# Kernel optimization log

Measured on AMD Instinct MI355X. Metric: run time of the kernel, lower is better.

Reference implementation:

```python
import jax, jax.numpy as jnp
import numpy as np

B, H, W, C = 32, 56, 56, 192
WS, SHIFT, HEADS = 7, 3, 6
HID = 4 * C
N = WS * WS
NW = (H // WS) * (W // WS)
EPS = 1e-5


def _rel_index():
    ch, cw = np.meshgrid(np.arange(WS), np.arange(WS), indexing='ij')
    coords = np.stack([ch.ravel(), cw.ravel()])  # [2, N]
    rel = coords[:, :, None] - coords[:, None, :]  # [2, N, N]
    rel = rel.transpose(1, 2, 0)
    rel[:, :, 0] += WS - 1
    rel[:, :, 1] += WS - 1
    rel[:, :, 0] *= 2 * WS - 1
    return rel.sum(-1).astype(np.int32)  # [N, N]


def _attn_mask():
    img = np.zeros((H, W), np.float32)
    sl = (slice(0, -WS), slice(-WS, -SHIFT), slice(-SHIFT, None))
    cnt = 0
    for hs in sl:
        for ws_ in sl:
            img[hs, ws_] = cnt
            cnt += 1
    mw = img.reshape(H // WS, WS, W // WS, WS).transpose(0, 2, 1, 3).reshape(-1, N)
    m = mw[:, None, :] - mw[:, :, None]
    return np.where(m != 0, -100.0, 0.0).astype(np.float32)  # [NW, N, N]


def setup_inputs() -> dict:
    key = jax.random.key(0)
    ks = jax.random.split(key, 16)
    r = lambda k, s, sc: (jax.random.normal(k, s, jnp.float32) * sc)
    return {
        'x': r(ks[0], (B, H * W, C), 1.0),
        'norm1_w': jnp.ones((C,), jnp.float32),
        'norm1_b': jnp.zeros((C,), jnp.float32),
        'qkv_w': r(ks[1], (C, 3 * C), 0.02),
        'qkv_b': jnp.zeros((3 * C,), jnp.float32),
        'bias_table': r(ks[2], ((2 * WS - 1) ** 2, HEADS), 0.02),
        'proj_w': r(ks[3], (C, C), 0.02),
        'proj_b': jnp.zeros((C,), jnp.float32),
        'norm2_w': jnp.ones((C,), jnp.float32),
        'norm2_b': jnp.zeros((C,), jnp.float32),
        'fc1_w': r(ks[4], (C, HID), 0.02),
        'fc1_b': jnp.zeros((HID,), jnp.float32),
        'fc2_w': r(ks[5], (HID, C), 0.02),
        'fc2_b': jnp.zeros((C,), jnp.float32),
        'attn_mask': jnp.asarray(_attn_mask()),
        'rel_index': jnp.asarray(_rel_index()),
    }


def _ln(x, w, b):
    mu = jnp.mean(x, -1, keepdims=True)
    var = jnp.mean(jnp.square(x - mu), -1, keepdims=True)
    return (x - mu) * jax.lax.rsqrt(var + EPS) * w + b


def reference(x, norm1_w, norm1_b, qkv_w, qkv_b, bias_table, proj_w, proj_b,
              norm2_w, norm2_b, fc1_w, fc1_b, fc2_w, fc2_b, attn_mask, rel_index):
    shortcut = x
    h = _ln(x, norm1_w, norm1_b).reshape(B, H, W, C)
    # cyclic shift
    h = jnp.roll(h, shift=(-SHIFT, -SHIFT), axis=(1, 2))
    # window partition -> (B*NW, N, C)
    h = h.reshape(B, H // WS, WS, W // WS, WS, C).transpose(0, 1, 3, 2, 4, 5)
    h = h.reshape(B * NW, N, C)
    # attention
    qkv = (h @ qkv_w + qkv_b).reshape(B * NW, N, 3, HEADS, C // HEADS)
    qkv = qkv.transpose(2, 0, 3, 1, 4)  # [3, B_, heads, N, d]
    q, k, v = qkv[0], qkv[1], qkv[2]
    scale = (C // HEADS) ** -0.5
    attn = jnp.einsum('bhnd,bhmd->bhnm', q * scale, k)
    bias = bias_table[rel_index].transpose(2, 0, 1)  # [heads, N, N]
    attn = attn + bias[None]
    attn = attn.reshape(B, NW, HEADS, N, N) + attn_mask[None, :, None]
    attn = jax.nn.softmax(attn.reshape(B * NW, HEADS, N, N), axis=-1)
    o = jnp.einsum('bhnm,bhmd->bhnd', attn, v)
    o = o.transpose(0, 2, 1, 3).reshape(B * NW, N, C)
    o = o @ proj_w + proj_b
    # window reverse
    o = o.reshape(B, H // WS, W // WS, WS, WS, C).transpose(0, 1, 3, 2, 4, 5)
    o = o.reshape(B, H, W, C)
    o = jnp.roll(o, shift=(SHIFT, SHIFT), axis=(1, 2)).reshape(B, H * W, C)
    x = shortcut + o
    # MLP (exact GELU, like torch nn.GELU)
    m = _ln(x, norm2_w, norm2_b)
    m = jax.nn.gelu(m @ fc1_w + fc1_b, approximate=False) @ fc2_w + fc2_b
    return x + m
```

## Files before the change

### kernel.cpp

```cpp
#include <hip/hip_runtime.h>
#include <math.h>

#define B_    32
#define HH    56
#define WW_   56
#define C_    192
#define WS_   7
#define SHIFT_ 3
#define HEADS_ 6
#define DH    32
#define N_    49
#define NWIN  2048
#define ROWS  100352
#define HID_  768
#define QKVN  576

typedef __bf16 bfr;
typedef __bf16 bf8 __attribute__((ext_vector_type(8)));
typedef float  f32x4 __attribute__((ext_vector_type(4)));

#define MFMA16(a,b,c) __builtin_amdgcn_mfma_f32_16x16x32_bf16(a,b,c,0,0,0)

#define OQW   0
#define OPW   110592
#define OW1   147456
#define OW2   294912
#define OBM   442368
#define WTOT  442368
#define BMTOT 1572864

__global__ __launch_bounds__(256) void k_prep(
    const float* __restrict__ qkvw, const float* __restrict__ projw,
    const float* __restrict__ w1,   const float* __restrict__ w2,
    bfr* __restrict__ wsp)
{
  int idx = blockIdx.x*256 + threadIdx.x;
  if (idx >= WTOT) return;
  if (idx < OPW)      { int i=idx;      int n=i/192, k=i%192; wsp[idx] = (bfr)qkvw[k*QKVN + n]; }
  else if (idx < OW1) { int i=idx-OPW;  int n=i/192, k=i%192; wsp[idx] = (bfr)projw[k*C_ + n]; }
  else if (idx < OW2) { int i=idx-OW1;  int n=i/192, k=i%192; wsp[idx] = (bfr)w1[k*HID_ + n]; }
  else                { int i=idx-OW2;  int n=i/768, k=i%768; wsp[idx] = (bfr)w2[k*C_ + n]; }
}

__global__ __launch_bounds__(256) void k_prep2(
    const float* __restrict__ btab, const int* __restrict__ rel,
    const float* __restrict__ mask, bfr* __restrict__ bm)
{
  int idx = blockIdx.x*256 + threadIdx.x;
  if (idx >= BMTOT) return;
  int col = idx & 63, row = (idx>>6) & 63, wi = (idx>>12) & 63, head = idx>>18;
  float v = -1e30f;
  if (row < N_ && col < N_) {
    int e = row*N_ + col;
    v = btab[rel[e]*HEADS_ + head] + mask[(size_t)wi*N_*N_ + e];
  }
  bm[idx] = (bfr)v;
}

#define SM_HS 0
#define SM_QS 25600
#define SM_KS 34816
#define SM_VT 44032
#define SM_P  53248
#define SM_OV 62464
#define SM_SR 67072
#define SM1_TOT 67328
#define HSP 200

__global__ __launch_bounds__(256) void k_attn(
    const float* __restrict__ x,
    const float* __restrict__ n1w, const float* __restrict__ n1b,
    const bfr*   __restrict__ wsp,
    const float* __restrict__ qkvb,
    const float* __restrict__ projb,
    float* __restrict__ out)
{
  __shared__ char smem[SM1_TOT];
  bfr*   hs    = (bfr*)(smem + SM_HS);
  bfr*   qs    = (bfr*)(smem + SM_QS);
  bfr*   ks    = (bfr*)(smem + SM_KS);
  bfr*   vT    = (bfr*)(smem + SM_VT);
  bfr*   P     = (bfr*)(smem + SM_P);
  bfr*   ov    = (bfr*)(smem + SM_OV);
  int*   srows = (int*)(smem + SM_SR);
  float* pj    = (float*)smem;

  const f32x4 ZERO4 = {0.f, 0.f, 0.f, 0.f};

  int win  = blockIdx.x;
  int tid  = threadIdx.x;
  int lane = tid & 63, wave = tid >> 6;
  int ln15 = lane & 15, quad = lane >> 4;
  int wi   = win & 63;

  if (tid < N_) {
    int bb = win >> 6;
    int wh = wi >> 3, ww = wi & 7;
    int th = tid / WS_, tw = tid % WS_;
    int sh = wh*WS_ + th + SHIFT_; if (sh >= HH) sh -= HH;
    int sw = ww*WS_ + tw + SHIFT_; if (sw >= WW_) sw -= WW_;
    srows[tid] = bb*HH*WW_ + sh*WW_ + sw;
  }
  {
    int* hz = (int*)hs;
    for (int i = tid; i < 64*HSP/2; i += 256) hz[i] = 0;
  }
  __syncthreads();
  for (int r = wave; r < N_; r += 4) {
    const float* xr = x + (size_t)srows[r]*C_;
    float v0 = xr[lane], v1 = xr[lane+64], v2 = xr[lane+128];
    float s = v0+v1+v2, q = v0*v0+v1*v1+v2*v2;
    #pragma unroll
    for (int m = 32; m; m >>= 1) { s += __shfl_xor(s, m); q += __shfl_xor(q, m); }
    float mu = s*(1.f/C_), var = q*(1.f/C_) - mu*mu;
    float rs = rsqrtf(var + 1e-5f);
    hs[r*HSP + lane]     = (bfr)((v0-mu)*rs*n1w[lane]     + n1b[lane]);
    hs[r*HSP + lane+64]  = (bfr)((v1-mu)*rs*n1w[lane+64]  + n1b[lane+64]);
    hs[r*HSP + lane+128] = (bfr)((v2-mu)*rs*n1w[lane+128] + n1b[lane+128]);
  }
  __syncthreads();

  const bfr* qkvwT  = wsp + OQW;
  const bfr* projwT = wsp + OPW;
  const bfr* bmask  = wsp + OBM;

  f32x4 accp[3][4];
  #pragma unroll
  for (int j=0;j<3;j++)
    #pragma unroll
    for (int mt=0;mt<4;mt++) accp[j][mt] = ZERO4;

  for (int pair = 0; pair < 3; pair++) {
    {
      f32x4 acc[3][4];
      #pragma unroll
      for (int j=0;j<3;j++)
        #pragma unroll
        for (int mt=0;mt<4;mt++) acc[j][mt] = ZERO4;
      for (int k0 = 0; k0 < C_; k0 += 32) {
        bf8 afr[4];
        #pragma unroll
        for (int mt=0;mt<4;mt++)
          afr[mt] = *(const bf8*)&hs[(mt*16+ln15)*HSP + k0 + quad*8];
        #pragma unroll
        for (int j=0;j<3;j++) {
          int colg = j*192 + pair*64 + wave*16 + ln15;
          bf8 bw = *(const bf8*)&qkvwT[(size_t)colg*192 + k0 + quad*8];
          #pragma unroll
          for (int mt=0;mt<4;mt++) acc[j][mt] = MFMA16(afr[mt], bw, acc[j][mt]);
        }
      }
      int colp = wave*16 + ln15;
      int hl = colp >> 5, d = colp & 31;
      #pragma unroll
      for (int j=0;j<3;j++) {
        float bias = qkvb[j*192 + pair*64 + colp];
        #pragma unroll
        for (int mt=0;mt<4;mt++)
          #pragma unroll
          for (int r=0;r<4;r++) {
            int row = mt*16 + quad*4 + r;
            float vv = acc[j][mt][r] + bias;
            if (j == 0)      qs[(hl*64+row)*36 + d] = (bfr)(vv*0.17677669529663689f);
            else if (j == 1) ks[(hl*64+row)*36 + d] = (bfr)vv;
            else             vT[(hl*32+d)*72 + row] = (bfr)vv;
          }
      }
    }
    __syncthreads();

    for (int hl = 0; hl < 2; hl++) {
      int head = pair*2 + hl;
      float val[4][4];
      {
        bf8 aq = *(const bf8*)&qs[(hl*64 + wave*16 + ln15)*36 + quad*8];
        #pragma unroll
        for (int nt = 0; nt < 4; nt++) {
          bf8 bk = *(const bf8*)&ks[(hl*64 + nt*16 + ln15)*36 + quad*8];
          f32x4 c = MFMA16(aq, bk, ZERO4);
          #pragma unroll
          for (int r=0;r<4;r++) val[nt][r] = c[r];
        }
      }
      {
        const bfr* bmh = bmask + (((size_t)head*64 + wi) << 12);
        #pragma unroll
        for (int nt=0;nt<4;nt++)
          #pragma unroll
          for (int r=0;r<4;r++)
            val[nt][r] += (float)bmh[(wave*16 + quad*4 + r)*64 + nt*16 + ln15];
      }
      {
        float mx[4], sum[4];
        #pragma unroll
        for (int r=0;r<4;r++) {
          mx[r] = fmaxf(fmaxf(val[0][r], val[1][r]), fmaxf(val[2][r], val[3][r]));
          #pragma unroll
          for (int m = 1; m < 16; m <<= 1) mx[r] = fmaxf(mx[r], __shfl_xor(mx[r], m));
        }
        #pragma unroll
        for (int nt=0;nt<4;nt++)
          #pragma unroll
          for (int r=0;r<4;r++) val[nt][r] = __expf(val[nt][r] - mx[r]);
        #pragma unroll
        for (int r=0;r<4;r++) {
          sum[r] = val[0][r] + val[1][r] + val[2][r] + val[3][r];
          #pragma unroll
          for (int m = 1; m < 16; m <<= 1) sum[r] += __shfl_xor(sum[r], m);
          sum[r] = 1.f / sum[r];
        }
        #pragma unroll
        for (int nt=0;nt<4;nt++)
          #pragma unroll
          for (int r=0;r<4;r++)
            P[(wave*16 + quad*4 + r)*72 + nt*16 + ln15] = (bfr)(val[nt][r]*sum[r]);
      }
      __syncthreads();
      #pragma unroll
      for (int nt = 0; nt < 2; nt++) {
        f32x4 c = ZERO4;
        #pragma unroll
        for (int k0 = 0; k0 < 64; k0 += 32) {
          bf8 ap = *(const bf8*)&P[(wave*16 + ln15)*72 + k0 + quad*8];
          bf8 bv = *(const bf8*)&vT[(hl*32 + nt*16 + ln15)*72 + k0 + quad*8];
          c = MFMA16(ap, bv, c);
        }
        #pragma unroll
        for (int r=0;r<4;r++)
          ov[(wave*16 + quad*4 + r)*36 + nt*16 + ln15] = (bfr)c[r];
      }
      __syncthreads();
      {
        bf8 afr[4];
        #pragma unroll
        for (int mt=0;mt<4;mt++)
          afr[mt] = *(const bf8*)&ov[(mt*16+ln15)*36 + quad*8];
        #pragma unroll
        for (int j=0;j<3;j++) {
          int col = (wave*3+j)*16 + ln15;
          bf8 bw = *(const bf8*)&projwT[(size_t)col*192 + head*32 + quad*8];
          #pragma unroll
          for (int mt=0;mt<4;mt++) accp[j][mt] = MFMA16(afr[mt], bw, accp[j][mt]);
        }
      }
    }
  }

  #pragma unroll
  for (int j=0;j<3;j++) {
    int col = (wave*3+j)*16 + ln15;
    float pb = projb[col];
    #pragma unroll
    for (int mt=0;mt<4;mt++)
      #pragma unroll
      for (int r=0;r<4;r++)
        pj[(mt*16 + quad*4 + r)*196 + col] = accp[j][mt][r] + pb;
  }
  __syncthreads();
  for (int idx = tid; idx < N_*C_; idx += 256) {
    int n = idx / C_, c = idx % C_;
    size_t gr = (size_t)srows[n]*C_ + c;
    out[gr] = x[gr] + pj[n*196 + c];
  }
}

#define SM2_TS  0
#define SM2_HID 25600
#define SM2_TOT 51200

__global__ __launch_bounds__(256, 3) void k_mlp(
    float* __restrict__ y,
    const float* __restrict__ n2w, const float* __restrict__ n2b,
    const bfr* __restrict__ wsp,
    const float* __restrict__ b1, const float* __restrict__ b2)
{
  __shared__ char smem[SM2_TOT];
  bfr*   ts   = (bfr*)(smem + SM2_TS);
  bfr*   hidc = (bfr*)(smem + SM2_HID);
  float* st   = (float*)smem;

  const f32x4 ZERO4 = {0.f, 0.f, 0.f, 0.f};

  int r0 = blockIdx.x * 64;
  int tid = threadIdx.x;
  int lane = tid & 63, wave = tid >> 6;
  int ln15 = lane & 15, quad = lane >> 4;

  for (int r = wave; r < 64; r += 4) {
    const float* yr = y + (size_t)(r0 + r)*C_;
    float v0 = yr[lane], v1 = yr[lane+64], v2 = yr[lane+128];
    float s = v0+v1+v2, q = v0*v0+v1*v1+v2*v2;
    #pragma unroll
    for (int m = 32; m; m >>= 1) { s += __shfl_xor(s, m); q += __shfl_xor(q, m); }
    float mu = s*(1.f/C_), var = q*(1.f/C_) - mu*mu;
    float rs = rsqrtf(var + 1e-5f);
    ts[r*HSP + lane]     = (bfr)((v0-mu)*rs*n2w[lane]     + n2b[lane]);
    ts[r*HSP + lane+64]  = (bfr)((v1-mu)*rs*n2w[lane+64]  + n2b[lane+64]);
    ts[r*HSP + lane+128] = (bfr)((v2-mu)*rs*n2w[lane+128] + n2b[lane+128]);
  }
  __syncthreads();

  const bfr* w1T = wsp + OW1;
  const bfr* w2T = wsp + OW2;

  f32x4 accp[3][4];
  #pragma unroll
  for (int j=0;j<3;j++)
    #pragma unroll
    for (int mt=0;mt<4;mt++) accp[j][mt] = ZERO4;

  for (int c = 0; c < 4; c++) {
    {
      f32x4 acc[3][4];
      #pragma unroll
      for (int j=0;j<3;j++)
        #pragma unroll
        for (int mt=0;mt<4;mt++) acc[j][mt] = ZERO4;
      for (int k0 = 0; k0 < C_; k0 += 32) {
        bf8 afr[4];
        #pragma unroll
        for (int mt=0;mt<4;mt++)
          afr[mt] = *(const bf8*)&ts[(mt*16+ln15)*HSP + k0 + quad*8];
        #pragma unroll
        for (int j=0;j<3;j++) {
          int gcol = (c*12 + wave*3 + j)*16 + ln15;
          bf8 bw = *(const bf8*)&w1T[(size_t)gcol*192 + k0 + quad*8];
          #pragma unroll
          for (int mt=0;mt<4;mt++) acc[j][mt] = MFMA16(afr[mt], bw, acc[j][mt]);
        }
      }
      #pragma unroll
      for (int j=0;j<3;j++) {
        int colc = (wave*3 + j)*16 + ln15;
        float bb = b1[c*192 + colc];
        #pragma unroll
        for (int mt=0;mt<4;mt++)
          #pragma unroll
          for (int r=0;r<4;r++) {
            int row = mt*16 + quad*4 + r;
            float g = acc[j][mt][r] + bb;
            float u = g*(1.5957691216f + 0.0713548170f*g*g);
            hidc[row*HSP + colc] = (bfr)(g / (1.f + __expf(-u)));
          }
      }
    }
    __syncthreads();
    for (int k0 = 0; k0 < 192; k0 += 32) {
      bf8 afr[4];
      #pragma unroll
      for (int mt=0;mt<4;mt++)
        afr[mt] = *(const bf8*)&hidc[(mt*16+ln15)*HSP + k0 + quad*8];
      #pragma unroll
      for (int j=0;j<3;j++) {
        int col = (wave*3+j)*16 + ln15;
        bf8 bw = *(const bf8*)&w2T[(size_t)col*768 + c*192 + k0 + quad*8];
        #pragma unroll
        for (int mt=0;mt<4;mt++) accp[j][mt] = MFMA16(afr[mt], bw, accp[j][mt]);
      }
    }
    __syncthreads();
  }

  #pragma unroll
  for (int j=0;j<3;j++) {
    int col = (wave*3+j)*16 + ln15;
    float bb = b2[col];
    #pragma unroll
    for (int mt=0;mt<4;mt++)
      #pragma unroll
      for (int r=0;r<4;r++) {
        int row = mt*16 + quad*4 + r;
        st[row*196 + col] = accp[j][mt][r] + bb;
      }
  }
  __syncthreads();
  for (int idx = tid; idx < 64*C_; idx += 256) {
    int r = idx / C_, c = idx % C_;
    size_t gr = (size_t)(r0 + r)*C_ + c;
    y[gr] = y[gr] + st[r*196 + c];
  }
}

extern "C" void kernel_launch(void* const* d_in, const int* in_sizes, int n_in,
                              void* d_out, int out_size, void* d_ws, size_t ws_size,
                              hipStream_t stream) {
  const float* x     = (const float*)d_in[0];
  const float* n1w   = (const float*)d_in[1];
  const float* n1b   = (const float*)d_in[2];
  const float* qkvw  = (const float*)d_in[3];
  const float* qkvb  = (const float*)d_in[4];
  const float* btab  = (const float*)d_in[5];
  const float* projw = (const float*)d_in[6];
  const float* projb = (const float*)d_in[7];
  const float* n2w   = (const float*)d_in[8];
  const float* n2b   = (const float*)d_in[9];
  const float* w1    = (const float*)d_in[10];
  const float* b1    = (const float*)d_in[11];
  const float* w2    = (const float*)d_in[12];
  const float* b2    = (const float*)d_in[13];
  const float* mask  = (const float*)d_in[14];
  const int*   rel   = (const int*)d_in[15];
  float* out = (float*)d_out;
  bfr*   wsp = (bfr*)d_ws;

  k_prep<<<(WTOT+255)/256, 256, 0, stream>>>(qkvw, projw, w1, w2, wsp);
  k_prep2<<<(BMTOT+255)/256, 256, 0, stream>>>(btab, rel, mask, wsp + OBM);
  k_attn<<<NWIN, 256, 0, stream>>>(x, n1w, n1b, wsp, qkvb, projb, out);
  k_mlp<<<ROWS/64, 256, 0, stream>>>(out, n2w, n2b, wsp, b1, b2);
}
```

Before: 572.0 us.

## Restructure window attention: fold bias-mask into MFMA accumulator and drop barriers

The bias+mask table is transposed in the prep kernel so each lane can load four contiguous bf16 values and use them as the initial accumulator of the QK^T MFMA, removing a separate scalar gather-and-add. Both heads of a pair are computed back to back. Per-head barriers are removed because each wave only reads the P rows it wrote itself. The per-head outputs go into a wider buffer so the projection runs after a single barrier. It also asks for two blocks per CU via launch bounds and zeroes only the padding rows of the LN buffer. In exchange it uses more shared memory and registers, which may limit occupancy or cause spills.

```diff
diff --git a/kernel.cpp b/kernel.cpp
--- a/kernel.cpp
+++ b/kernel.cpp
@@ -17,6 +17,7 @@
 
 typedef __bf16 bfr;
 typedef __bf16 bf8 __attribute__((ext_vector_type(8)));
+typedef __bf16 bf4 __attribute__((ext_vector_type(4)));
 typedef float  f32x4 __attribute__((ext_vector_type(4)));
 
 #define MFMA16(a,b,c) __builtin_amdgcn_mfma_f32_16x16x32_bf16(a,b,c,0,0,0)
@@ -48,7 +49,7 @@
 {
   int idx = blockIdx.x*256 + threadIdx.x;
   if (idx >= BMTOT) return;
-  int col = idx & 63, row = (idx>>6) & 63, wi = (idx>>12) & 63, head = idx>>18;
+  int row = idx & 63, col = (idx>>6) & 63, wi = (idx>>12) & 63, head = idx>>18;
   float v = -1e30f;
   if (row < N_ && col < N_) {
     int e = row*N_ + col;
@@ -63,11 +64,11 @@
 #define SM_VT 44032
 #define SM_P  53248
 #define SM_OV 62464
-#define SM_SR 67072
-#define SM1_TOT 67328
+#define SM_SR 71680
+#define SM1_TOT 71936
 #define HSP 200
 
-__global__ __launch_bounds__(256) void k_attn(
+__global__ __launch_bounds__(256, 2) void k_attn(
     const float* __restrict__ x,
     const float* __restrict__ n1w, const float* __restrict__ n1b,
     const bfr*   __restrict__ wsp,
@@ -81,7 +82,7 @@
   bfr*   ks    = (bfr*)(smem + SM_KS);
   bfr*   vT    = (bfr*)(smem + SM_VT);
   bfr*   P     = (bfr*)(smem + SM_P);
-  bfr*   ov    = (bfr*)(smem + SM_OV);
+  bfr*   ov2   = (bfr*)(smem + SM_OV);
   int*   srows = (int*)(smem + SM_SR);
   float* pj    = (float*)smem;
 
@@ -102,8 +103,8 @@
     srows[tid] = bb*HH*WW_ + sh*WW_ + sw;
   }
   {
-    int* hz = (int*)hs;
-    for (int i = tid; i < 64*HSP/2; i += 256) hz[i] = 0;
+    int* hz = (int*)(hs + 49*HSP);
+    for (int i = tid; i < 15*HSP/2; i += 256) hz[i] = 0;
   }
   __syncthreads();
   for (int r = wave; r < N_; r += 4) {
@@ -169,53 +170,50 @@
     }
     __syncthreads();
 
+    float val[2][4][4];
+    #pragma unroll
     for (int hl = 0; hl < 2; hl++) {
       int head = pair*2 + hl;
-      float val[4][4];
-      {
-        bf8 aq = *(const bf8*)&qs[(hl*64 + wave*16 + ln15)*36 + quad*8];
-        #pragma unroll
-        for (int nt = 0; nt < 4; nt++) {
-          bf8 bk = *(const bf8*)&ks[(hl*64 + nt*16 + ln15)*36 + quad*8];
-          f32x4 c = MFMA16(aq, bk, ZERO4);
-          #pragma unroll
-          for (int r=0;r<4;r++) val[nt][r] = c[r];
-        }
-      }
-      {
-        const bfr* bmh = bmask + (((size_t)head*64 + wi) << 12);
-        #pragma unroll
-        for (int nt=0;nt<4;nt++)
-          #pragma unroll
-          for (int r=0;r<4;r++)
-            val[nt][r] += (float)bmh[(wave*16 + quad*4 + r)*64 + nt*16 + ln15];
-      }
-      {
-        float mx[4], sum[4];
-        #pragma unroll
-        for (int r=0;r<4;r++) {
-          mx[r] = fmaxf(fmaxf(val[0][r], val[1][r]), fmaxf(val[2][r], val[3][r]));
-          #pragma unroll
-          for (int m = 1; m < 16; m <<= 1) mx[r] = fmaxf(mx[r], __shfl_xor(mx[r], m));
-        }
-        #pragma unroll
-        for (int nt=0;nt<4;nt++)
-          #pragma unroll
-          for (int r=0;r<4;r++) val[nt][r] = __expf(val[nt][r] - mx[r]);
-        #pragma unroll
-        for (int r=0;r<4;r++) {
-          sum[r] = val[0][r] + val[1][r] + val[2][r] + val[3][r];
-          #pragma unroll
-          for (int m = 1; m < 16; m <<= 1) sum[r] += __shfl_xor(sum[r], m);
-          sum[r] = 1.f / sum[r];
-        }
-        #pragma unroll
-        for (int nt=0;nt<4;nt++)
-          #pragma unroll
-          for (int r=0;r<4;r++)
-            P[(wave*16 + quad*4 + r)*72 + nt*16 + ln15] = (bfr)(val[nt][r]*sum[r]);
-      }
-      __syncthreads();
+      const bfr* bmh = bmask + (((size_t)head*64 + wi) << 12);
+      bf8 aq = *(const bf8*)&qs[(hl*64 + wave*16 + ln15)*36 + quad*8];
+      #pragma unroll
+      for (int nt = 0; nt < 4; nt++) {
+        bf4 bm4 = *(const bf4*)&bmh[(nt*16 + ln15)*64 + wave*16 + quad*4];
+        f32x4 c;
+        c[0] = (float)bm4[0]; c[1] = (float)bm4[1];
+        c[2] = (float)bm4[2]; c[3] = (float)bm4[3];
+        bf8 bk = *(const bf8*)&ks[(hl*64 + nt*16 + ln15)*36 + quad*8];
+        c = MFMA16(aq, bk, c);
+        #pragma unroll
+        for (int r=0;r<4;r++) val[hl][nt][r] = c[r];
+      }
+    }
+
+    #pragma unroll
+    for (int hl = 0; hl < 2; hl++) {
+      float mx[4], sum[4];
+      #pragma unroll
+      for (int r=0;r<4;r++) {
+        mx[r] = fmaxf(fmaxf(val[hl][0][r], val[hl][1][r]), fmaxf(val[hl][2][r], val[hl][3][r]));
+        #pragma unroll
+        for (int m = 1; m < 16; m <<= 1) mx[r] = fmaxf(mx[r], __shfl_xor(mx[r], m));
+      }
+      #pragma unroll
+      for (int nt=0;nt<4;nt++)
+        #pragma unroll
+        for (int r=0;r<4;r++) val[hl][nt][r] = __expf(val[hl][nt][r] - mx[r]);
+      #pragma unroll
+      for (int r=0;r<4;r++) {
+        sum[r] = val[hl][0][r] + val[hl][1][r] + val[hl][2][r] + val[hl][3][r];
+        #pragma unroll
+        for (int m = 1; m < 16; m <<= 1) sum[r] += __shfl_xor(sum[r], m);
+        sum[r] = 1.f / sum[r];
+      }
+      #pragma unroll
+      for (int nt=0;nt<4;nt++)
+        #pragma unroll
+        for (int r=0;r<4;r++)
+          P[(wave*16 + quad*4 + r)*72 + nt*16 + ln15] = (bfr)(val[hl][nt][r]*sum[r]);
       #pragma unroll
       for (int nt = 0; nt < 2; nt++) {
         f32x4 c = ZERO4;
@@ -227,25 +225,29 @@
         }
         #pragma unroll
         for (int r=0;r<4;r++)
-          ov[(wave*16 + quad*4 + r)*36 + nt*16 + ln15] = (bfr)c[r];
-      }
-      __syncthreads();
-      {
-        bf8 afr[4];
-        #pragma unroll
-        for (int mt=0;mt<4;mt++)
-          afr[mt] = *(const bf8*)&ov[(mt*16+ln15)*36 + quad*8];
-        #pragma unroll
-        for (int j=0;j<3;j++) {
-          int col = (wave*3+j)*16 + ln15;
-          bf8 bw = *(const bf8*)&projwT[(size_t)col*192 + head*32 + quad*8];
-          #pragma unroll
-          for (int mt=0;mt<4;mt++) accp[j][mt] = MFMA16(afr[mt], bw, accp[j][mt]);
-        }
-      }
-    }
-  }
-
+          ov2[(wave*16 + quad*4 + r)*72 + hl*36 + nt*16 + ln15] = (bfr)c[r];
+      }
+    }
+    __syncthreads();
+
+    #pragma unroll
+    for (int hl = 0; hl < 2; hl++) {
+      int head = pair*2 + hl;
+      bf8 afr[4];
+      #pragma unroll
+      for (int mt=0;mt<4;mt++)
+        afr[mt] = *(const bf8*)&ov2[(mt*16+ln15)*72 + hl*36 + quad*8];
+      #pragma unroll
+      for (int j=0;j<3;j++) {
+        int col = (wave*3+j)*16 + ln15;
+        bf8 bw = *(const bf8*)&projwT[(size_t)col*192 + head*32 + quad*8];
+        #pragma unroll
+        for (int mt=0;mt<4;mt++) accp[j][mt] = MFMA16(afr[mt], bw, accp[j][mt]);
+      }
+    }
+  }
+
+  __syncthreads();
   #pragma unroll
   for (int j=0;j<3;j++) {
     int col = (wave*3+j)*16 + ln15;
```

New measurement: 535.6 us. 1.07x faster.

## Double block size to 512 threads, process both heads concurrently, split MLP K across waves

Applied to the files above, without the earlier changes.

Both attention and MLP kernels move to 512-thread blocks. In attention, the two heads of each pair are handled by separate wave groups at the same time. The bias+mask table is transposed so it can be loaded as bf4 vectors and used as the MFMA accumulator seed, which removes one sync per head. In the MLP, hidden chunks widen to 384 columns and the fc2 K range is split across two wave halves, whose partial sums are combined in shared memory. This trades larger LDS use (about 78-79KB per block) for more waves per block and fewer barriers, which may limit how many blocks fit per CU.

```diff
diff --git a/kernel.cpp b/kernel.cpp
--- a/kernel.cpp
+++ b/kernel.cpp
@@ -17,6 +17,7 @@
 
 typedef __bf16 bfr;
 typedef __bf16 bf8 __attribute__((ext_vector_type(8)));
+typedef __bf16 bf4 __attribute__((ext_vector_type(4)));
 typedef float  f32x4 __attribute__((ext_vector_type(4)));
 
 #define MFMA16(a,b,c) __builtin_amdgcn_mfma_f32_16x16x32_bf16(a,b,c,0,0,0)
@@ -48,7 +49,7 @@
 {
   int idx = blockIdx.x*256 + threadIdx.x;
   if (idx >= BMTOT) return;
-  int col = idx & 63, row = (idx>>6) & 63, wi = (idx>>12) & 63, head = idx>>18;
+  int row = idx & 63, col = (idx>>6) & 63, wi = (idx>>12) & 63, head = idx>>18;
   float v = -1e30f;
   if (row < N_ && col < N_) {
     int e = row*N_ + col;
@@ -57,17 +58,17 @@
   bm[idx] = (bfr)v;
 }
 
+#define HSP   196
 #define SM_HS 0
-#define SM_QS 25600
-#define SM_KS 34816
-#define SM_VT 44032
-#define SM_P  53248
-#define SM_OV 62464
-#define SM_SR 67072
-#define SM1_TOT 67328
-#define HSP 200
-
-__global__ __launch_bounds__(256) void k_attn(
+#define SM_QS 25088
+#define SM_KS 34304
+#define SM_VT 43520
+#define SM_P  52736
+#define SM_OV 70144
+#define SM_SR 79360
+#define SM1_TOT 79616
+
+__global__ __launch_bounds__(512, 4) void k_attn(
     const float* __restrict__ x,
     const float* __restrict__ n1w, const float* __restrict__ n1b,
     const bfr*   __restrict__ wsp,
@@ -80,8 +81,8 @@
   bfr*   qs    = (bfr*)(smem + SM_QS);
   bfr*   ks    = (bfr*)(smem + SM_KS);
   bfr*   vT    = (bfr*)(smem + SM_VT);
-  bfr*   P     = (bfr*)(smem + SM_P);
-  bfr*   ov    = (bfr*)(smem + SM_OV);
+  bfr*   P2    = (bfr*)(smem + SM_P);
+  bfr*   ov2   = (bfr*)(smem + SM_OV);
   int*   srows = (int*)(smem + SM_SR);
   float* pj    = (float*)smem;
 
@@ -91,6 +92,7 @@
   int tid  = threadIdx.x;
   int lane = tid & 63, wave = tid >> 6;
   int ln15 = lane & 15, quad = lane >> 4;
+  int rt   = wave & 3, hl = wave >> 2;
   int wi   = win & 63;
 
   if (tid < N_) {
@@ -102,11 +104,11 @@
     srows[tid] = bb*HH*WW_ + sh*WW_ + sw;
   }
   {
-    int* hz = (int*)hs;
-    for (int i = tid; i < 64*HSP/2; i += 256) hz[i] = 0;
-  }
-  __syncthreads();
-  for (int r = wave; r < N_; r += 4) {
+    int* hz = (int*)(hs + 49*HSP);
+    for (int i = tid; i < 15*HSP/2; i += 512) hz[i] = 0;
+  }
+  __syncthreads();
+  for (int r = wave; r < N_; r += 8) {
     const float* xr = x + (size_t)srows[r]*C_;
     float v0 = xr[lane], v1 = xr[lane+64], v2 = xr[lane+128];
     float s = v0+v1+v2, q = v0*v0+v1*v1+v2*v2;
@@ -132,132 +134,154 @@
 
   for (int pair = 0; pair < 3; pair++) {
     {
-      f32x4 acc[3][4];
+      float qb[3];
+      #pragma unroll
+      for (int j=0;j<3;j++) qb[j] = qkvb[j*192 + pair*64 + rt*16 + ln15];
+      f32x4 acc[3][2];
       #pragma unroll
       for (int j=0;j<3;j++)
         #pragma unroll
-        for (int mt=0;mt<4;mt++) acc[j][mt] = ZERO4;
-      for (int k0 = 0; k0 < C_; k0 += 32) {
-        bf8 afr[4];
-        #pragma unroll
-        for (int mt=0;mt<4;mt++)
-          afr[mt] = *(const bf8*)&hs[(mt*16+ln15)*HSP + k0 + quad*8];
+        for (int mtl=0;mtl<2;mtl++) acc[j][mtl] = ZERO4;
+      #pragma unroll
+      for (int kk = 0; kk < 6; kk++) {
+        bf8 afr[2];
+        #pragma unroll
+        for (int mtl=0;mtl<2;mtl++)
+          afr[mtl] = *(const bf8*)&hs[((hl*2+mtl)*16+ln15)*HSP + kk*32 + quad*8];
         #pragma unroll
         for (int j=0;j<3;j++) {
-          int colg = j*192 + pair*64 + wave*16 + ln15;
-          bf8 bw = *(const bf8*)&qkvwT[(size_t)colg*192 + k0 + quad*8];
+          bf8 bw = *(const bf8*)&qkvwT[(size_t)(j*192 + pair*64 + rt*16 + ln15)*192
+                                       + kk*32 + quad*8];
           #pragma unroll
-          for (int mt=0;mt<4;mt++) acc[j][mt] = MFMA16(afr[mt], bw, acc[j][mt]);
+          for (int mtl=0;mtl<2;mtl++) acc[j][mtl] = MFMA16(afr[mtl], bw, acc[j][mtl]);
         }
       }
-      int colp = wave*16 + ln15;
-      int hl = colp >> 5, d = colp & 31;
+      int colp = rt*16 + ln15;
+      int chl = colp >> 5, d = colp & 31;
       #pragma unroll
       for (int j=0;j<3;j++) {
-        float bias = qkvb[j*192 + pair*64 + colp];
-        #pragma unroll
-        for (int mt=0;mt<4;mt++)
+        #pragma unroll
+        for (int mtl=0;mtl<2;mtl++)
           #pragma unroll
           for (int r=0;r<4;r++) {
-            int row = mt*16 + quad*4 + r;
-            float vv = acc[j][mt][r] + bias;
-            if (j == 0)      qs[(hl*64+row)*36 + d] = (bfr)(vv*0.17677669529663689f);
-            else if (j == 1) ks[(hl*64+row)*36 + d] = (bfr)vv;
-            else             vT[(hl*32+d)*72 + row] = (bfr)vv;
+            int row = (hl*2+mtl)*16 + quad*4 + r;
+            float vv = acc[j][mtl][r] + qb[j];
+            if (j == 0)      qs[(chl*64+row)*36 + d] = (bfr)(vv*0.17677669529663689f);
+            else if (j == 1) ks[(chl*64+row)*36 + d] = (bfr)vv;
+            else             vT[(chl*32+d)*72 + row] = (bfr)vv;
           }
       }
     }
     __syncthreads();
 
-    for (int hl = 0; hl < 2; hl++) {
-      int head = pair*2 + hl;
-      float val[4][4];
-      {
-        bf8 aq = *(const bf8*)&qs[(hl*64 + wave*16 + ln15)*36 + quad*8];
-        #pragma unroll
-        for (int nt = 0; nt < 4; nt++) {
-          bf8 bk = *(const bf8*)&ks[(hl*64 + nt*16 + ln15)*36 + quad*8];
-          f32x4 c = MFMA16(aq, bk, ZERO4);
-          #pragma unroll
-          for (int r=0;r<4;r++) val[nt][r] = c[r];
-        }
-      }
-      {
-        const bfr* bmh = bmask + (((size_t)head*64 + wi) << 12);
-        #pragma unroll
-        for (int nt=0;nt<4;nt++)
-          #pragma unroll
-          for (int r=0;r<4;r++)
-            val[nt][r] += (float)bmh[(wave*16 + quad*4 + r)*64 + nt*16 + ln15];
-      }
-      {
-        float mx[4], sum[4];
-        #pragma unroll
-        for (int r=0;r<4;r++) {
-          mx[r] = fmaxf(fmaxf(val[0][r], val[1][r]), fmaxf(val[2][r], val[3][r]));
-          #pragma unroll
-          for (int m = 1; m < 16; m <<= 1) mx[r] = fmaxf(mx[r], __shfl_xor(mx[r], m));
-        }
-        #pragma unroll
-        for (int nt=0;nt<4;nt++)
-          #pragma unroll
-          for (int r=0;r<4;r++) val[nt][r] = __expf(val[nt][r] - mx[r]);
-        #pragma unroll
-        for (int r=0;r<4;r++) {
-          sum[r] = val[0][r] + val[1][r] + val[2][r] + val[3][r];
-          #pragma unroll
-          for (int m = 1; m < 16; m <<= 1) sum[r] += __shfl_xor(sum[r], m);
-          sum[r] = 1.f / sum[r];
-        }
-        #pragma unroll
-        for (int nt=0;nt<4;nt++)
-          #pragma unroll
-          for (int r=0;r<4;r++)
-            P[(wave*16 + quad*4 + r)*72 + nt*16 + ln15] = (bfr)(val[nt][r]*sum[r]);
-      }
-      __syncthreads();
+    int head = pair*2 + hl;
+    bf4 bm4[4];
+    {
+      const bfr* bmh = bmask + (((size_t)head*64 + wi) << 12);
+      #pragma unroll
+      for (int nt = 0; nt < 4; nt++)
+        bm4[nt] = *(const bf4*)&bmh[(nt*16 + ln15)*64 + rt*16 + quad*4];
+    }
+
+    float val[4][4];
+    {
+      bf8 aq = *(const bf8*)&qs[(hl*64 + rt*16 + ln15)*36 + quad*8];
+      #pragma unroll
+      for (int nt = 0; nt < 4; nt++) {
+        f32x4 c;
+        c[0] = (float)bm4[nt][0]; c[1] = (float)bm4[nt][1];
+        c[2] = (float)bm4[nt][2]; c[3] = (float)bm4[nt][3];
+        bf8 bk = *(const bf8*)&ks[(hl*64 + nt*16 + ln15)*36 + quad*8];
+        c = MFMA16(aq, bk, c);
+        #pragma unroll
+        for (int r=0;r<4;r++) val[nt][r] = c[r];
+      }
+    }
+
+    bf8 pw[3];
+    #pragma unroll
+    for (int j = 0; j < 3; j++)
+      pw[j] = *(const bf8*)&projwT[(size_t)((rt*3+j)*16 + ln15)*192 + head*32 + quad*8];
+
+    {
+      float mx[4], sum[4];
+      #pragma unroll
+      for (int r=0;r<4;r++) {
+        mx[r] = fmaxf(fmaxf(val[0][r], val[1][r]), fmaxf(val[2][r], val[3][r]));
+        #pragma unroll
+        for (int m = 1; m < 16; m <<= 1) mx[r] = fmaxf(mx[r], __shfl_xor(mx[r], m));
+      }
+      #pragma unroll
+      for (int nt=0;nt<4;nt++)
+        #pragma unroll
+        for (int r=0;r<4;r++) val[nt][r] = __expf(val[nt][r] - mx[r]);
+      #pragma unroll
+      for (int r=0;r<4;r++) {
+        sum[r] = val[0][r] + val[1][r] + val[2][r] + val[3][r];
+        #pragma unroll
+        for (int m = 1; m < 16; m <<= 1) sum[r] += __shfl_xor(sum[r], m);
+        sum[r] = 1.f / sum[r];
+      }
+      #pragma unroll
+      for (int nt=0;nt<4;nt++)
+        #pragma unroll
+        for (int r=0;r<4;r++)
+          P2[(hl*64 + rt*16 + quad*4 + r)*68 + nt*16 + ln15] = (bfr)(val[nt][r]*sum[r]);
       #pragma unroll
       for (int nt = 0; nt < 2; nt++) {
         f32x4 c = ZERO4;
         #pragma unroll
         for (int k0 = 0; k0 < 64; k0 += 32) {
-          bf8 ap = *(const bf8*)&P[(wave*16 + ln15)*72 + k0 + quad*8];
+          bf8 ap = *(const bf8*)&P2[(hl*64 + rt*16 + ln15)*68 + k0 + quad*8];
           bf8 bv = *(const bf8*)&vT[(hl*32 + nt*16 + ln15)*72 + k0 + quad*8];
           c = MFMA16(ap, bv, c);
         }
         #pragma unroll
         for (int r=0;r<4;r++)
-          ov[(wave*16 + quad*4 + r)*36 + nt*16 + ln15] = (bfr)c[r];
-      }
-      __syncthreads();
-      {
-        bf8 afr[4];
-        #pragma unroll
-        for (int mt=0;mt<4;mt++)
-          afr[mt] = *(const bf8*)&ov[(mt*16+ln15)*36 + quad*8];
-        #pragma unroll
-        for (int j=0;j<3;j++) {
-          int col = (wave*3+j)*16 + ln15;
-          bf8 bw = *(const bf8*)&projwT[(size_t)col*192 + head*32 + quad*8];
-          #pragma unroll
-          for (int mt=0;mt<4;mt++) accp[j][mt] = MFMA16(afr[mt], bw, accp[j][mt]);
-        }
-      }
-    }
-  }
-
-  #pragma unroll
-  for (int j=0;j<3;j++) {
-    int col = (wave*3+j)*16 + ln15;
-    float pb = projb[col];
-    #pragma unroll
-    for (int mt=0;mt<4;mt++)
-      #pragma unroll
-      for (int r=0;r<4;r++)
-        pj[(mt*16 + quad*4 + r)*196 + col] = accp[j][mt][r] + pb;
-  }
-  __syncthreads();
-  for (int idx = tid; idx < N_*C_; idx += 256) {
+          ov2[(rt*16 + quad*4 + r)*72 + hl*36 + nt*16 + ln15] = (bfr)c[r];
+      }
+    }
+    __syncthreads();
+
+    {
+      bf8 afr[4];
+      #pragma unroll
+      for (int mt=0;mt<4;mt++)
+        afr[mt] = *(const bf8*)&ov2[(mt*16+ln15)*72 + hl*36 + quad*8];
+      #pragma unroll
+      for (int j=0;j<3;j++)
+        #pragma unroll
+        for (int mt=0;mt<4;mt++) accp[j][mt] = MFMA16(afr[mt], pw[j], accp[j][mt]);
+    }
+  }
+
+  __syncthreads();
+  if (hl == 0) {
+    #pragma unroll
+    for (int j=0;j<3;j++) {
+      int col = (rt*3+j)*16 + ln15;
+      float pb = projb[col];
+      #pragma unroll
+      for (int mt=0;mt<4;mt++)
+        #pragma unroll
+        for (int r=0;r<4;r++)
+          pj[(mt*16 + quad*4 + r)*196 + col] = accp[j][mt][r] + pb;
+    }
+  }
+  __syncthreads();
+  if (hl == 1) {
+    #pragma unroll
+    for (int j=0;j<3;j++) {
+      int col = (rt*3+j)*16 + ln15;
+      #pragma unroll
+      for (int mt=0;mt<4;mt++)
+        #pragma unroll
+        for (int r=0;r<4;r++)
+          pj[(mt*16 + quad*4 + r)*196 + col] += accp[j][mt][r];
+    }
+  }
+  __syncthreads();
+  for (int idx = tid; idx < N_*C_; idx += 512) {
     int n = idx / C_, c = idx % C_;
     size_t gr = (size_t)srows[n]*C_ + c;
     out[gr] = x[gr] + pj[n*196 + c];
@@ -265,10 +289,10 @@
 }
 
 #define SM2_TS  0
-#define SM2_HID 25600
-#define SM2_TOT 51200
-
-__global__ __launch_bounds__(256, 3) void k_mlp(
+#define SM2_HID 25088
+#define SM2_TOT 75264
+
+__global__ __launch_bounds__(512, 4) void k_mlp(
     float* __restrict__ y,
     const float* __restrict__ n2w, const float* __restrict__ n2b,
     const bfr* __restrict__ wsp,
@@ -285,8 +309,9 @@
   int tid = threadIdx.x;
   int lane = tid & 63, wave = tid >> 6;
   int ln15 = lane & 15, quad = lane >> 4;
-
-  for (int r = wave; r < 64; r += 4) {
+  int cg = wave & 3, kh = wave >> 2;
+
+  for (int r = wave; r < 64; r += 8) {
     const float* yr = y + (size_t)(r0 + r)*C_;
     float v0 = yr[lane], v1 = yr[lane+64], v2 = yr[lane+128];
     float s = v0+v1+v2, q = v0*v0+v1*v1+v2*v2;
@@ -309,51 +334,55 @@
     #pragma unroll
     for (int mt=0;mt<4;mt++) accp[j][mt] = ZERO4;
 
-  for (int c = 0; c < 4; c++) {
+  for (int c = 0; c < 2; c++) {
     {
       f32x4 acc[3][4];
       #pragma unroll
       for (int j=0;j<3;j++)
         #pragma unroll
         for (int mt=0;mt<4;mt++) acc[j][mt] = ZERO4;
-      for (int k0 = 0; k0 < C_; k0 += 32) {
+      float bb[3];
+      #pragma unroll
+      for (int j=0;j<3;j++) bb[j] = b1[c*384 + wave*48 + j*16 + ln15];
+      #pragma unroll
+      for (int kk = 0; kk < 6; kk++) {
         bf8 afr[4];
         #pragma unroll
         for (int mt=0;mt<4;mt++)
-          afr[mt] = *(const bf8*)&ts[(mt*16+ln15)*HSP + k0 + quad*8];
+          afr[mt] = *(const bf8*)&ts[(mt*16+ln15)*HSP + kk*32 + quad*8];
         #pragma unroll
         for (int j=0;j<3;j++) {
-          int gcol = (c*12 + wave*3 + j)*16 + ln15;
-          bf8 bw = *(const bf8*)&w1T[(size_t)gcol*192 + k0 + quad*8];
+          bf8 bw = *(const bf8*)&w1T[(size_t)(c*384 + wave*48 + j*16 + ln15)*192
+                                     + kk*32 + quad*8];
           #pragma unroll
           for (int mt=0;mt<4;mt++) acc[j][mt] = MFMA16(afr[mt], bw, acc[j][mt]);
         }
       }
       #pragma unroll
       for (int j=0;j<3;j++) {
-        int colc = (wave*3 + j)*16 + ln15;
-        float bb = b1[c*192 + colc];
+        int colc = wave*48 + j*16 + ln15;
         #pragma unroll
         for (int mt=0;mt<4;mt++)
           #pragma unroll
           for (int r=0;r<4;r++) {
             int row = mt*16 + quad*4 + r;
-            float g = acc[j][mt][r] + bb;
+            float g = acc[j][mt][r] + bb[j];
             float u = g*(1.5957691216f + 0.0713548170f*g*g);
-            hidc[row*HSP + colc] = (bfr)(g / (1.f + __expf(-u)));
+            hidc[row*392 + colc] = (bfr)(g / (1.f + __expf(-u)));
           }
       }
     }
     __syncthreads();
-    for (int k0 = 0; k0 < 192; k0 += 32) {
+    #pragma unroll
+    for (int kk = 0; kk < 6; kk++) {
       bf8 afr[4];
       #pragma unroll
       for (int mt=0;mt<4;mt++)
-        afr[mt] = *(const bf8*)&hidc[(mt*16+ln15)*HSP + k0 + quad*8];
+        afr[mt] = *(const bf8*)&hidc[(mt*16+ln15)*392 + kh*192 + kk*32 + quad*8];
       #pragma unroll
       for (int j=0;j<3;j++) {
-        int col = (wave*3+j)*16 + ln15;
-        bf8 bw = *(const bf8*)&w2T[(size_t)col*768 + c*192 + k0 + quad*8];
+        bf8 bw = *(const bf8*)&w2T[(size_t)((cg*3+j)*16 + ln15)*768
+                                   + c*384 + kh*192 + kk*32 + quad*8];
         #pragma unroll
         for (int mt=0;mt<4;mt++) accp[j][mt] = MFMA16(afr[mt], bw, accp[j][mt]);
       }
@@ -361,20 +390,32 @@
     __syncthreads();
   }
 
-  #pragma unroll
-  for (int j=0;j<3;j++) {
-    int col = (wave*3+j)*16 + ln15;
-    float bb = b2[col];
-    #pragma unroll
-    for (int mt=0;mt<4;mt++)
-      #pragma unroll
-      for (int r=0;r<4;r++) {
-        int row = mt*16 + quad*4 + r;
-        st[row*196 + col] = accp[j][mt][r] + bb;
-      }
-  }
-  __syncthreads();
-  for (int idx = tid; idx < 64*C_; idx += 256) {
+  if (kh == 0) {
+    #pragma unroll
+    for (int j=0;j<3;j++) {
+      int col = (cg*3+j)*16 + ln15;
+      float bb2 = b2[col];
+      #pragma unroll
+      for (int mt=0;mt<4;mt++)
+        #pragma unroll
+        for (int r=0;r<4;r++)
+          st[(mt*16 + quad*4 + r)*196 + col] = accp[j][mt][r] + bb2;
+    }
+  }
+  __syncthreads();
+  if (kh == 1) {
+    #pragma unroll
+    for (int j=0;j<3;j++) {
+      int col = (cg*3+j)*16 + ln15;
+      #pragma unroll
+      for (int mt=0;mt<4;mt++)
+        #pragma unroll
+        for (int r=0;r<4;r++)
+          st[(mt*16 + quad*4 + r)*196 + col] += accp[j][mt][r];
+    }
+  }
+  __syncthreads();
+  for (int idx = tid; idx < 64*C_; idx += 512) {
     int r = idx / C_, c = idx % C_;
     size_t gr = (size_t)(r0 + r)*C_ + c;
     y[gr] = y[gr] + st[r*196 + c];
@@ -405,6 +446,6 @@
 
   k_prep<<<(WTOT+255)/256, 256, 0, stream>>>(qkvw, projw, w1, w2, wsp);
   k_prep2<<<(BMTOT+255)/256, 256, 0, stream>>>(btab, rel, mask, wsp + OBM);
-  k_attn<<<NWIN, 256, 0, stream>>>(x, n1w, n1b, wsp, qkvb, projb, out);
-  k_mlp<<<ROWS/64, 256, 0, stream>>>(out, n2w, n2b, wsp, b1, b2);
+  k_attn<<<NWIN, 512, 0, stream>>>(x, n1w, n1b, wsp, qkvb, projb, out);
+  k_mlp<<<ROWS/64, 512, 0, stream>>>(out, n2w, n2b, wsp, b1, b2);
 }
```

After: 622.6 us. 8.9% more time.
